# Performance work log

Hardware: AMD Instinct MI355X
Metric: run time of the kernel (lower is better)

The kernel has to match this reference:

```python
import jax, jax.numpy as jnp
import numpy as np

ROPE_BASE = 10000.0


def _rope(x):
    # Faithful to the torch module: positions indexed by x.shape[2],
    # which after split_heads is the HEADS axis. x: [B, S, H, D]
    B, S, H, D = x.shape
    theta = 1.0 / (ROPE_BASE ** (jnp.arange(0, D, 2, dtype=x.dtype) / D))  # [D/2]
    pos = jnp.arange(H, dtype=x.dtype)[:, None]  # [H, 1]
    ang = pos * theta  # [H, D/2], broadcasts against [B, S, H, D/2]
    sin, cos = jnp.sin(ang), jnp.cos(ang)
    xe, xo = x[..., 0::2], x[..., 1::2]
    re = xe * cos - xo * sin
    ro = xe * sin + xo * cos
    # interleave back: even slots <- re, odd slots <- ro
    return jnp.stack([re, ro], axis=-1).reshape(B, S, H, D)


def setup_inputs() -> dict:
    key = jax.random.key(0)
    k0, k1, k2, k3 = jax.random.split(key, 4)
    B, S, Dm = 8, 2048, 2048
    scale = 1.0 / np.sqrt(Dm)
    return {
        "x": jax.random.normal(k0, (B, S, Dm), dtype=jnp.float32),
        "Wq": jax.random.normal(k1, (Dm, Dm), dtype=jnp.float32) * scale,
        "Wk": jax.random.normal(k2, (Dm, Dm), dtype=jnp.float32) * scale,
        "Wv": jax.random.normal(k3, (Dm, Dm), dtype=jnp.float32) * scale,
        "st_pos": 0,
    }


def reference(x, Wq, Wk, Wv, st_pos):
    B, S, Dm = x.shape
    H = 16
    D = Dm // H  # head_dim = 128
    q = jnp.einsum("bsd,df->bsf", x, Wq).reshape(B, S, H, D)
    k = jnp.einsum("bsd,df->bsf", x, Wk).reshape(B, S, H, D)
    v = jnp.einsum("bsd,df->bsf", x, Wv).reshape(B, S, H, D)
    q = _rope(q)
    k = _rope(k)
    return q, k, v
```

## Files before the change

kernel.cpp:

```cpp
#include <hip/hip_runtime.h>
#include <hip/hip_bf16.h>
#include <stdint.h>


typedef __attribute__((ext_vector_type(8))) short short8;
typedef __attribute__((ext_vector_type(4))) float f32x4;

__device__ __forceinline__ unsigned short f2bf(float f) {
  __bf16 h = (__bf16)f;
  return __builtin_bit_cast(unsigned short, h);
}

__device__ __forceinline__ void gload_lds16(const void* g, void* l) {
  __builtin_amdgcn_global_load_lds((const __attribute__((address_space(1))) void*)g,
                                   (__attribute__((address_space(3))) void*)l,
                                   16, 0, 0);
}


__global__ __launch_bounds__(256) void convert_x(const float* __restrict__ X,
                                                 unsigned short* __restrict__ Xb,
                                                 int n8) {
  const int stride = gridDim.x * blockDim.x;
  for (int i = blockIdx.x * blockDim.x + threadIdx.x; i < n8; i += stride) {
    const float4 v0 = ((const float4*)X)[(size_t)i * 2 + 0];
    const float4 v1 = ((const float4*)X)[(size_t)i * 2 + 1];
    uint4 w;
    w.x = (uint32_t)f2bf(v0.x) | ((uint32_t)f2bf(v0.y) << 16);
    w.y = (uint32_t)f2bf(v0.z) | ((uint32_t)f2bf(v0.w) << 16);
    w.z = (uint32_t)f2bf(v1.x) | ((uint32_t)f2bf(v1.y) << 16);
    w.w = (uint32_t)f2bf(v1.z) | ((uint32_t)f2bf(v1.w) << 16);
    ((uint4*)Xb)[i] = w;
  }
}

__global__ __launch_bounds__(256) void transpose_cvt3(const float* __restrict__ W0,
                                                      const float* __restrict__ W1,
                                                      const float* __restrict__ W2,
                                                      unsigned short* __restrict__ WT) {
  __shared__ unsigned short tile[64][65];
  const int z = blockIdx.z;
  const float* W = (z == 0) ? W0 : (z == 1) ? W1 : W2;
  unsigned short* WTz = WT + (size_t)z * 2048 * 2048;
  const int bx = blockIdx.x * 64;
  const int by = blockIdx.y * 64;
  const int t  = threadIdx.x;
  const int tr = t >> 4;
  const int tc = (t & 15) * 4;
#pragma unroll
  for (int i = 0; i < 4; ++i) {
    const int r = tr + i * 16;
    const float4 v = *(const float4*)&W[(size_t)(by + r) * 2048 + bx + tc];
    tile[r][tc + 0] = f2bf(v.x);
    tile[r][tc + 1] = f2bf(v.y);
    tile[r][tc + 2] = f2bf(v.z);
    tile[r][tc + 3] = f2bf(v.w);
  }
  __syncthreads();
#pragma unroll
  for (int i = 0; i < 4; ++i) {
    const int a = tr + i * 16;
    ushort4 o;
    o.x = tile[tc + 0][a];
    o.y = tile[tc + 1][a];
    o.z = tile[tc + 2][a];
    o.w = tile[tc + 3][a];
    *(ushort4*)&WTz[(size_t)(bx + a) * 2048 + by + tc] = o;
  }
}


__global__ __launch_bounds__(512, 2) void qkv_fused13(const unsigned short* __restrict__ Xb,
                                                      const unsigned short* __restrict__ WT,
                                                      float* __restrict__ Out) {
  extern __shared__ char smem[];

  const int wg  = blockIdx.x;
  const int swz = (wg & 7) * 192 + (wg >> 3);
  const int mb  = swz / 24, nb = swz % 24;
  const int m0  = mb * 256, n0 = nb * 256;

  const int tid  = threadIdx.x;
  const int wave = tid >> 6, lane = tid & 63;
  const int l15  = lane & 15, lg = lane >> 4;
  const int wm   = (wave >> 2) * 128;
  const int wn   = (wave & 3) * 64;
  const int s0   = ((lg ^ (l15 & 7)) << 4);

  const unsigned short* Xp = Xb + (size_t)m0 * 2048;
  const unsigned short* Wp = WT + (size_t)n0 * 2048;

  const int srow  = tid >> 3;
  const int sslot = tid & 7;

  f32x4 acc[8][4] = {};

#define GLD_A(TP1, H)                                                         \
  do {                                                                        \
    char* dst_ = smem + (((TP1) & 1) << 16) + ((H) << 14);                    \
    _Pragma("unroll") for (int i_ = 0; i_ < 2; ++i_) {                        \
      const int row_ = (H) * 128 + i_ * 64 + srow;                            \
      gload_lds16(Xp + (size_t)row_ * 2048 + (TP1) * 64 +                     \
                      ((sslot ^ (row_ & 7)) << 3),                            \
                  dst_ + i_ * 8192 + tid * 16);                               \
    }                                                                         \
  } while (0)

#define GLD_B(TP2, H)                                                         \
  do {                                                                        \
    char* dst_ = smem + (((TP2) & 1) << 16) + 32768 + ((H) << 14);            \
    _Pragma("unroll") for (int i_ = 0; i_ < 2; ++i_) {                        \
      const int row_ = (H) * 128 + i_ * 64 + srow;                            \
      gload_lds16(Wp + (size_t)row_ * 2048 + (TP2) * 64 +                     \
                      ((sslot ^ (row_ & 7)) << 3),                            \
                  dst_ + i_ * 8192 + tid * 16);                               \
    }                                                                         \
  } while (0)

#define LDA4(DST, MH, KS)                                                     \
  _Pragma("unroll") for (int mi_ = 0; mi_ < 4; ++mi_)                         \
      (DST)[mi_] = *(const short8*)(Ab +                                      \
          ((wm + (MH) * 64 + mi_ * 16 + l15) << 7) + (s0 ^ ((KS) << 6)));

#define LDB4(DST, KS)                                                         \
  _Pragma("unroll") for (int ni_ = 0; ni_ < 4; ++ni_)                         \
      (DST)[ni_] = *(const short8*)(Bb +                                      \
          ((wn + ni_ * 16 + l15) << 7) + (s0 ^ ((KS) << 6)));

#define MFMA16(MH, AR, BR)                                                    \
  do {                                                                        \
    __builtin_amdgcn_s_setprio(1);                                            \
    _Pragma("unroll") for (int mi_ = 0; mi_ < 4; ++mi_)                       \
      _Pragma("unroll") for (int ni_ = 0; ni_ < 4; ++ni_)                     \
        asm("v_mfma_f32_16x16x32_bf16 %0, %1, %2, %0"                         \
            : "+v"(acc[(MH) * 4 + mi_][ni_])                                  \
            : "v"((AR)[mi_]), "v"((BR)[ni_]));                                \
    __builtin_amdgcn_s_setprio(0);                                            \
  } while (0)

  GLD_A(0, 0); GLD_A(0, 1);
  GLD_B(0, 0); GLD_B(0, 1);
  GLD_B(1, 0); GLD_B(1, 1);
  asm volatile("s_waitcnt vmcnt(4)" ::: "memory");
  __builtin_amdgcn_s_barrier();

  for (int t = 0; t < 32; ++t) {
    const char* Ab = smem + ((t & 1) << 16);
    const char* Bb = Ab + 32768;
    short8 a0[4], a1[4], b0[4], b1[4];

    LDB4(b0, 0);
    LDB4(b1, 1);
    LDA4(a0, 0, 0);
    asm volatile("s_waitcnt lgkmcnt(0)" ::: "memory");
    __builtin_amdgcn_s_barrier();
    LDA4(a1, 1, 0);
    if (t < 31) GLD_A(t + 1, 0);
    MFMA16(0, a0, b0);
    LDA4(a0, 0, 1);
    if (t < 31) GLD_A(t + 1, 1);
    MFMA16(1, a1, b0);
    LDA4(a1, 1, 1);
    if (t < 30) GLD_B(t + 2, 0);
    MFMA16(0, a0, b1);
    if (t < 30) GLD_B(t + 2, 1);
    MFMA16(1, a1, b1);
    if (t == 30)     asm volatile("s_waitcnt vmcnt(0)" ::: "memory");
    else if (t < 30) asm volatile("s_waitcnt vmcnt(4)" ::: "memory");
    __builtin_amdgcn_s_barrier();
  }

#undef GLD_A
#undef GLD_B
#undef LDA4
#undef LDB4
#undef MFMA16

#pragma unroll
  for (int ni = 0; ni < 4; ++ni) {
    const int col = n0 + wn + ni * 16 + l15;
    const int sec = col >> 11;
    const int lc  = col & 2047;
    float c = 1.0f, ssg = 0.0f;
    if (sec < 2) {
      const int h = lc >> 7;
      const int p = (lc & 127) >> 1;
      const float theta = exp2f(-(float)p * 0.20762050593046014f);
      float s;
      sincosf((float)h * theta, &s, &c);
      ssg = (l15 & 1) ? s : -s;
    }
    float* outp = Out + (size_t)sec * 33554432 + lc;
#pragma unroll
    for (int mi = 0; mi < 8; ++mi) {
      const f32x4 a = acc[mi][ni];
#pragma unroll
      for (int r = 0; r < 4; ++r) {
        const float val = a[r];
        float res = val;
        if (sec < 2) {
          const float other = __shfl_xor(val, 1);
          res = val * c + other * ssg;
        }
        __builtin_nontemporal_store(
            res, outp + (size_t)(m0 + wm + mi * 16 + lg * 4 + r) * 2048);
      }
    }
  }
}

__global__ __launch_bounds__(256) void qkv_gemm_small(const float* __restrict__ X,
                                                      const unsigned short* __restrict__ WTl,
                                                      float* __restrict__ Out,
                                                      const int do_rope) {
  __shared__ unsigned short As[128 * 64];
  __shared__ unsigned short Bs[128 * 64];
  const int t    = threadIdx.x;
  const int wave = t >> 6, lane = t & 63;
  const int l15  = lane & 15, lg = lane >> 4;
  const int wm   = (wave >> 1) * 64;
  const int wn   = (wave & 1) * 64;
  const int m0   = blockIdx.y * 128;
  const int n0   = blockIdx.x * 128;

  f32x4 acc[4][4] = {};

  for (int kt = 0; kt < 2048; kt += 64) {
#pragma unroll
    for (int i = 0; i < 8; ++i) {
      const int f = i * 256 + t;
      const int row = f >> 4, chunk = f & 15;
      const float4 v = *(const float4*)&X[(size_t)(m0 + row) * 2048 + kt + chunk * 4];
      const uint32_t lo = (uint32_t)f2bf(v.x) | ((uint32_t)f2bf(v.y) << 16);
      const uint32_t hi = (uint32_t)f2bf(v.z) | ((uint32_t)f2bf(v.w) << 16);
      const int slot = chunk >> 1;
      const int off  = row * 128 + (((slot ^ (row & 7)) << 4) | ((chunk & 1) << 3));
      uint2* p = (uint2*)((char*)As + off);
      p->x = lo; p->y = hi;
    }
#pragma unroll
    for (int i = 0; i < 4; ++i) {
      const int seg = i * 4 + wave;
      const int row = seg * 8 + (lane >> 3);
      const int ps  = lane & 7;
      const int ss  = ps ^ (row & 7);
      gload_lds16(WTl + (size_t)(n0 + row) * 2048 + kt + ss * 8,
                  (char*)Bs + seg * 1024 + lane * 16);
    }
    __syncthreads();
#pragma unroll
    for (int kk = 0; kk < 2; ++kk) {
      short8 afr[4], bfr[4];
#pragma unroll
      for (int mi = 0; mi < 4; ++mi) {
        const int row  = wm + mi * 16 + l15;
        const int slot = kk * 4 + lg;
        afr[mi] = *(const short8*)((const char*)As + row * 128 + ((slot ^ (row & 7)) << 4));
      }
#pragma unroll
      for (int ni = 0; ni < 4; ++ni) {
        const int row  = wn + ni * 16 + l15;
        const int slot = kk * 4 + lg;
        bfr[ni] = *(const short8*)((const char*)Bs + row * 128 + ((slot ^ (row & 7)) << 4));
      }
#pragma unroll
      for (int mi = 0; mi < 4; ++mi)
#pragma unroll
        for (int ni = 0; ni < 4; ++ni)
          asm("v_mfma_f32_16x16x32_bf16 %0, %1, %2, %0"
              : "+v"(acc[mi][ni])
              : "v"(afr[mi]), "v"(bfr[ni]));
    }
    __syncthreads();
  }

#pragma unroll
  for (int ni = 0; ni < 4; ++ni) {
    const int col = n0 + wn + ni * 16 + l15;
    float c = 1.0f, ssg = 0.0f;
    if (do_rope) {
      const int h = col >> 7;
      const int p = (col & 127) >> 1;
      const float theta = exp2f(-(float)p * 0.20762050593046014f);
      float s;
      sincosf((float)h * theta, &s, &c);
      ssg = (l15 & 1) ? s : -s;
    }
#pragma unroll
    for (int mi = 0; mi < 4; ++mi) {
      const f32x4 a = acc[mi][ni];
#pragma unroll
      for (int r = 0; r < 4; ++r) {
        const float val = a[r];
        float res = val;
        if (do_rope) {
          const float other = __shfl_xor(val, 1);
          res = val * c + other * ssg;
        }
        Out[(size_t)(m0 + wm + mi * 16 + lg * 4 + r) * 2048 + col] = res;
      }
    }
  }
}

extern "C" void kernel_launch(void* const* d_in, const int* in_sizes, int n_in,
                              void* d_out, int out_size, void* d_ws, size_t ws_size,
                              hipStream_t stream) {
  (void)in_sizes; (void)n_in; (void)out_size;
  const float* x  = (const float*)d_in[0];
  const float* Wq = (const float*)d_in[1];
  const float* Wk = (const float*)d_in[2];
  const float* Wv = (const float*)d_in[3];
  float* out = (float*)d_out;

  const size_t XB_ELEMS = 16384ull * 2048;
  const size_t WT_ELEMS = 6144ull * 2048;

  if (ws_size >= (XB_ELEMS + WT_ELEMS) * sizeof(unsigned short)) {
    unsigned short* Xb  = (unsigned short*)d_ws;
    unsigned short* WTf = Xb + XB_ELEMS;
    convert_x<<<2048, 256, 0, stream>>>(x, Xb, (int)(XB_ELEMS / 8));
    transpose_cvt3<<<dim3(32, 32, 3), 256, 0, stream>>>(Wq, Wk, Wv, WTf);
    hipFuncSetAttribute((const void*)qkv_fused13,
                        hipFuncAttributeMaxDynamicSharedMemorySize, 131072);
    qkv_fused13<<<1536, 512, 131072, stream>>>(Xb, WTf, out);
  } else {
    unsigned short* WqT = (unsigned short*)d_ws;
    unsigned short* WkT = WqT + 2048ull * 2048;
    unsigned short* WvT = WkT + 2048ull * 2048;
    dim3 tb(256), tg(32, 32);
    transpose_cvt3<<<dim3(32, 32, 1), 256, 0, stream>>>(Wq, Wq, Wq, WqT);
    transpose_cvt3<<<dim3(32, 32, 1), 256, 0, stream>>>(Wk, Wk, Wk, WkT);
    transpose_cvt3<<<dim3(32, 32, 1), 256, 0, stream>>>(Wv, Wv, Wv, WvT);
    dim3 gg(16, 128);
    qkv_gemm_small<<<gg, tb, 0, stream>>>(x, WqT, out,            1);
    qkv_gemm_small<<<gg, tb, 0, stream>>>(x, WkT, out + 33554432, 1);
    qkv_gemm_small<<<gg, tb, 0, stream>>>(x, WvT, out + 67108864, 0);
  }
}
```

Before: 436.3 us.

## Load B operand directly from global into registers, stage only A in LDS

Stops staging the weight (B) tile through LDS. Each wave now loads its B fragments straight from global memory into registers, one k-tile ahead, while A alone stays double-buffered in a 64KB static LDS array. The aim is to cut LDS traffic and size so more workgroups can fit per CU, and to drop one barrier per iteration. The cost is uncoalesced-ish per-lane global loads for B that are reused only within each wave, so the same B data is fetched four times per workgroup. The vmcnt(4) waits may also no longer match the mix of outstanding loads.

```diff
diff --git a/kernel.cpp b/kernel.cpp
--- a/kernel.cpp
+++ b/kernel.cpp
@@ -70,10 +70,10 @@
 }
 
 
-__global__ __launch_bounds__(512, 2) void qkv_fused13(const unsigned short* __restrict__ Xb,
+__global__ __launch_bounds__(512, 2) void qkv_fused14(const unsigned short* __restrict__ Xb,
                                                       const unsigned short* __restrict__ WT,
                                                       float* __restrict__ Out) {
-  extern __shared__ char smem[];
+  __shared__ char smemA[2][32768];
 
   const int wg  = blockIdx.x;
   const int swz = (wg & 7) * 192 + (wg >> 3);
@@ -88,44 +88,33 @@
   const int s0   = ((lg ^ (l15 & 7)) << 4);
 
   const unsigned short* Xp = Xb + (size_t)m0 * 2048;
-  const unsigned short* Wp = WT + (size_t)n0 * 2048;
+  const unsigned short* Bp = WT + (size_t)(n0 + wn + l15) * 2048 + lg * 8;
 
   const int srow  = tid >> 3;
   const int sslot = tid & 7;
 
   f32x4 acc[8][4] = {};
 
-#define GLD_A(TP1, H)                                                         \
+#define GLD_A(TP1)                                                            \
   do {                                                                        \
-    char* dst_ = smem + (((TP1) & 1) << 16) + ((H) << 14);                    \
-    _Pragma("unroll") for (int i_ = 0; i_ < 2; ++i_) {                        \
-      const int row_ = (H) * 128 + i_ * 64 + srow;                            \
+    char* dst_ = &smemA[0][0] + (((TP1) & 1) << 15);                          \
+    _Pragma("unroll") for (int i_ = 0; i_ < 4; ++i_) {                        \
+      const int row_ = i_ * 64 + srow;                                        \
       gload_lds16(Xp + (size_t)row_ * 2048 + (TP1) * 64 +                     \
                       ((sslot ^ (row_ & 7)) << 3),                            \
                   dst_ + i_ * 8192 + tid * 16);                               \
     }                                                                         \
   } while (0)
 
-#define GLD_B(TP2, H)                                                         \
-  do {                                                                        \
-    char* dst_ = smem + (((TP2) & 1) << 16) + 32768 + ((H) << 14);            \
-    _Pragma("unroll") for (int i_ = 0; i_ < 2; ++i_) {                        \
-      const int row_ = (H) * 128 + i_ * 64 + srow;                            \
-      gload_lds16(Wp + (size_t)row_ * 2048 + (TP2) * 64 +                     \
-                      ((sslot ^ (row_ & 7)) << 3),                            \
-                  dst_ + i_ * 8192 + tid * 16);                               \
-    }                                                                         \
-  } while (0)
+#define LDB4G(DST, KT, KS)                                                    \
+  _Pragma("unroll") for (int ni_ = 0; ni_ < 4; ++ni_)                         \
+      (DST)[ni_] = *(const short8*)(Bp + (size_t)ni_ * 32768 + (KT) +         \
+                                    (KS) * 32);
 
 #define LDA4(DST, MH, KS)                                                     \
   _Pragma("unroll") for (int mi_ = 0; mi_ < 4; ++mi_)                         \
       (DST)[mi_] = *(const short8*)(Ab +                                      \
           ((wm + (MH) * 64 + mi_ * 16 + l15) << 7) + (s0 ^ ((KS) << 6)));
-
-#define LDB4(DST, KS)                                                         \
-  _Pragma("unroll") for (int ni_ = 0; ni_ < 4; ++ni_)                         \
-      (DST)[ni_] = *(const short8*)(Bb +                                      \
-          ((wn + ni_ * 16 + l15) << 7) + (s0 ^ ((KS) << 6)));
 
 #define MFMA16(MH, AR, BR)                                                    \
   do {                                                                        \
@@ -138,43 +127,46 @@
     __builtin_amdgcn_s_setprio(0);                                            \
   } while (0)
 
-  GLD_A(0, 0); GLD_A(0, 1);
-  GLD_B(0, 0); GLD_B(0, 1);
-  GLD_B(1, 0); GLD_B(1, 1);
+#define TILE(T, BCUR, BNXT, DO_STAGE)                                         \
+  do {                                                                        \
+    const char* Ab = &smemA[0][0] + (((T) & 1) << 15);                        \
+    short8 a0[4], a1[4], bc1[4];                                              \
+    LDB4G(bc1, (T) * 64, 1);                     \
+    if (DO_STAGE) GLD_A((T) + 1);                                             \
+    LDA4(a0, 0, 0);                                                           \
+    LDA4(a1, 1, 0);                                                           \
+    MFMA16(0, a0, BCUR);                                              \
+    LDA4(a0, 0, 1);                                                           \
+    MFMA16(1, a1, BCUR);                            \
+    if (DO_STAGE) LDB4G(BNXT, ((T) + 1) * 64, 0);                             \
+    LDA4(a1, 1, 1);                                                           \
+    MFMA16(0, a0, bc1);                                               \
+    MFMA16(1, a1, bc1);                                               \
+    if (DO_STAGE) {                                                           \
+      asm volatile("s_waitcnt vmcnt(4)" ::: "memory");                        \
+      __builtin_amdgcn_s_barrier();                                           \
+    }                                                                         \
+  } while (0)
+
+  short8 bA[4], bB[4];
+
+  GLD_A(0);
+  LDB4G(bA, 0, 0);
   asm volatile("s_waitcnt vmcnt(4)" ::: "memory");
   __builtin_amdgcn_s_barrier();
 
-  for (int t = 0; t < 32; ++t) {
-    const char* Ab = smem + ((t & 1) << 16);
-    const char* Bb = Ab + 32768;
-    short8 a0[4], a1[4], b0[4], b1[4];
-
-    LDB4(b0, 0);
-    LDB4(b1, 1);
-    LDA4(a0, 0, 0);
-    asm volatile("s_waitcnt lgkmcnt(0)" ::: "memory");
-    __builtin_amdgcn_s_barrier();
-    LDA4(a1, 1, 0);
-    if (t < 31) GLD_A(t + 1, 0);
-    MFMA16(0, a0, b0);
-    LDA4(a0, 0, 1);
-    if (t < 31) GLD_A(t + 1, 1);
-    MFMA16(1, a1, b0);
-    LDA4(a1, 1, 1);
-    if (t < 30) GLD_B(t + 2, 0);
-    MFMA16(0, a0, b1);
-    if (t < 30) GLD_B(t + 2, 1);
-    MFMA16(1, a1, b1);
-    if (t == 30)     asm volatile("s_waitcnt vmcnt(0)" ::: "memory");
-    else if (t < 30) asm volatile("s_waitcnt vmcnt(4)" ::: "memory");
-    __builtin_amdgcn_s_barrier();
-  }
+  for (int tt = 0; tt < 15; ++tt) {
+    TILE(2 * tt,     bA, bB, 1);
+    TILE(2 * tt + 1, bB, bA, 1);
+  }
+  TILE(30, bA, bB, 1);
+  TILE(31, bB, bA, 0);
 
 #undef GLD_A
-#undef GLD_B
+#undef LDB4G
 #undef LDA4
-#undef LDB4
 #undef MFMA16
+#undef TILE
 
 #pragma unroll
   for (int ni = 0; ni < 4; ++ni) {
@@ -321,9 +313,7 @@
     unsigned short* WTf = Xb + XB_ELEMS;
     convert_x<<<2048, 256, 0, stream>>>(x, Xb, (int)(XB_ELEMS / 8));
     transpose_cvt3<<<dim3(32, 32, 3), 256, 0, stream>>>(Wq, Wk, Wv, WTf);
-    hipFuncSetAttribute((const void*)qkv_fused13,
-                        hipFuncAttributeMaxDynamicSharedMemorySize, 131072);
-    qkv_fused13<<<1536, 512, 131072, stream>>>(Xb, WTf, out);
+    qkv_fused14<<<1536, 512, 0, stream>>>(Xb, WTf, out);
   } else {
     unsigned short* WqT = (unsigned short*)d_ws;
     unsigned short* WkT = WqT + 2048ull * 2048;
```

Result: slower. 503.7 us (+15.4%).
